# Kernel tuning notes

Hardware: AMD Instinct MI355X
Metric: run time of the kernel (lower is better)

## Reference

```python
import jax, jax.numpy as jnp
import numpy as np

DIM = 768
NUM_HEADS = 8
SCALE = (DIM // NUM_HEADS) ** -0.5  # 96^-0.5, matches head_dim**-0.5
B, N = 8, 4096


def setup_inputs() -> dict:
    key = jax.random.key(0)
    k1, k2 = jax.random.split(key)
    x_1 = jax.random.normal(k1, (B, N, DIM), dtype=jnp.float32)
    x_2 = jax.random.normal(k2, (B, N, DIM), dtype=jnp.float32)
    return {"x_1": x_1, "x_2": x_2}


def reference(x_1, x_2):
    # q = x_1, k = v = x_2; channel-wise (transpose) attention
    # attn[b,c,d] = sum_n q[b,n,c] * k[b,n,d] * scale   -> [B, C, C]
    attn = jnp.einsum('bnc,bnd->bcd', x_1, x_2) * SCALE
    attn = jax.nn.softmax(attn, axis=-1)
    # out[b,c,n] = sum_d attn[b,c,d] * v[b,n,d]          -> [B, C, N]
    return jnp.einsum('bcd,bnd->bcn', attn, x_2)
```

## Files before the change

kernel.cpp:

```cpp
#include <hip/hip_runtime.h>
#include <stdint.h>

typedef _Float16 f16;
typedef _Float16 f16x4 __attribute__((ext_vector_type(4)));
typedef _Float16 f16x8 __attribute__((ext_vector_type(8)));
typedef float f32x4 __attribute__((ext_vector_type(4)));

#define NB 8
#define NN 4096
#define CC 768
#define SCALE_F 0.10206207261596577f

#define GLDS16(gp, lp)                                                       \
  __builtin_amdgcn_global_load_lds(                                          \
      (__attribute__((address_space(1))) void*)(gp),                         \
      (__attribute__((address_space(3))) void*)(lp), 16, 0, 0)

__global__ __launch_bounds__(256) void k_convert(
    const float* __restrict__ x1, const float* __restrict__ x2,
    f16* __restrict__ x1t, f16* __restrict__ x2t, f16* __restrict__ x2b) {
  __shared__ float tile[64][65];
  const int which = blockIdx.z >> 3;
  const int b = blockIdx.z & 7;
  const int n0 = blockIdx.x << 6;
  const int c0 = blockIdx.y << 6;
  const float* src = (which ? x2 : x1) + (size_t)b * NN * CC;
  f16* dt = (which ? x2t : x1t) + (size_t)b * CC * NN;
  const int t = threadIdx.x;
  const int rowi = t >> 4;
  const int col4 = (t & 15) << 2;
#pragma unroll
  for (int it = 0; it < 4; ++it) {
    const int r = it * 16 + rowi;
    const float4 v =
        *reinterpret_cast<const float4*>(&src[(size_t)(n0 + r) * CC + c0 + col4]);
    tile[r][col4 + 0] = v.x;
    tile[r][col4 + 1] = v.y;
    tile[r][col4 + 2] = v.z;
    tile[r][col4 + 3] = v.w;
    if (which) {
      f16x4 o = {(f16)v.x, (f16)v.y, (f16)v.z, (f16)v.w};
      *reinterpret_cast<f16x4*>(
          &x2b[(size_t)b * NN * CC + (size_t)(n0 + r) * CC + c0 + col4]) = o;
    }
  }
  __syncthreads();
  const int c = t >> 2;
  const int nb = (t & 3) << 4;
  f16x8 lo, hi;
#pragma unroll
  for (int j = 0; j < 8; ++j) lo[j] = (f16)tile[nb + j][c];
#pragma unroll
  for (int j = 0; j < 8; ++j) hi[j] = (f16)tile[nb + 8 + j][c];
  f16* o = &dt[(size_t)(c0 + c) * NN + n0 + nb];
  *reinterpret_cast<f16x8*>(o) = lo;
  *reinterpret_cast<f16x8*>(o + 8) = hi;
}

template <bool ATOMIC, int SWZ>
__global__ __launch_bounds__(256) void k_gemm_bt(
    const f16* __restrict__ A, const f16* __restrict__ B,
    float* __restrict__ C, int klen, int lda, int ldb, int ldc,
    size_t sA, size_t sB, size_t sC) {
  __shared__ __align__(16) f16 As[2][128 * 32];
  __shared__ __align__(16) f16 Bs[2][128 * 32];

  const int lin = blockIdx.x;
  const int xcd = lin & 7;
  const int slot = lin >> 3;
  int bx, by, b, ks;
  if (SWZ == 1) {
    b = xcd;
    ks = slot / 36;
    const int item = slot % 36;
    bx = item % 6;
    by = item / 6;
  } else {
    b = xcd;
    ks = 0;
    bx = slot / 6;
    by = slot % 6;
  }

  const f16* Ap = A + (size_t)b * sA + (size_t)by * 128 * lda + (size_t)ks * klen;
  const f16* Bp = B + (size_t)b * sB + (size_t)bx * 128 * ldb + (size_t)ks * klen;
  float* Cp = C + (size_t)b * sC + (size_t)by * 128 * ldc + bx * 128;

  const int tid = threadIdx.x;
  const int wave = tid >> 6;
  const int lane = tid & 63;
  const int wr = wave >> 1;
  const int wc = wave & 1;

  const f16* ga0 = Ap + (size_t)(wave * 32 + (lane >> 2)) * lda + (lane & 3) * 8;
  const f16* ga1 = ga0 + (size_t)16 * lda;
  const f16* gb0 = Bp + (size_t)(wave * 32 + (lane >> 2)) * ldb + (lane & 3) * 8;
  const f16* gb1 = gb0 + (size_t)16 * ldb;
  const int lofs0 = wave * 32 * 32;
  const int lofs1 = lofs0 + 16 * 32;

  const int raofs = (wr * 64 + (lane & 15)) * 32 + (lane >> 4) * 8;
  const int rbofs = (wc * 64 + (lane & 15)) * 32 + (lane >> 4) * 8;

  f32x4 acc[4][4] = {};

  const int nit = klen >> 5;
  GLDS16(ga0, &As[0][lofs0]);
  GLDS16(ga1, &As[0][lofs1]);
  GLDS16(gb0, &Bs[0][lofs0]);
  GLDS16(gb1, &Bs[0][lofs1]);

  for (int it = 0; it < nit; ++it) {
    const int cur = it & 1;
    const int nxt = cur ^ 1;
    __syncthreads();
    if (it + 1 < nit) {
      ga0 += 32; ga1 += 32; gb0 += 32; gb1 += 32;
      GLDS16(ga0, &As[nxt][lofs0]);
      GLDS16(ga1, &As[nxt][lofs1]);
      GLDS16(gb0, &Bs[nxt][lofs0]);
      GLDS16(gb1, &Bs[nxt][lofs1]);
    }
    const f16* ra = &As[cur][raofs];
    const f16* rb = &Bs[cur][rbofs];
    f16x8 af[4], bfv[4];
#pragma unroll
    for (int i = 0; i < 4; ++i)
      af[i] = *reinterpret_cast<const f16x8*>(ra + i * 16 * 32);
#pragma unroll
    for (int j = 0; j < 4; ++j)
      bfv[j] = *reinterpret_cast<const f16x8*>(rb + j * 16 * 32);
#pragma unroll
    for (int i = 0; i < 4; ++i)
#pragma unroll
      for (int j = 0; j < 4; ++j)
        acc[i][j] = __builtin_amdgcn_mfma_f32_16x16x32_f16(af[i], bfv[j],
                                                           acc[i][j], 0, 0, 0);
  }

  const int col = lane & 15;
  const int rq = (lane >> 4) * 4;
#pragma unroll
  for (int i = 0; i < 4; ++i) {
    const int r0 = wr * 64 + i * 16 + rq;
#pragma unroll
    for (int j = 0; j < 4; ++j) {
      const int cidx = wc * 64 + j * 16 + col;
#pragma unroll
      for (int r = 0; r < 4; ++r) {
        const float v = acc[i][j][r];
        if (ATOMIC)
          atomicAdd(&Cp[(size_t)(r0 + r) * ldc + cidx], v);
        else
          Cp[(size_t)(r0 + r) * ldc + cidx] = v;
      }
    }
  }
}

__global__ __launch_bounds__(256) void k_softmax(const float* __restrict__ S,
                                                 f16* __restrict__ P) {
  const int row = blockIdx.x * 4 + (threadIdx.x >> 6);
  const int lane = threadIdx.x & 63;
  const float* s = S + (size_t)row * CC;
  float v[12];
#pragma unroll
  for (int j = 0; j < 3; ++j) {
    const float4 t = *reinterpret_cast<const float4*>(&s[j * 256 + lane * 4]);
    v[j * 4 + 0] = t.x * SCALE_F;
    v[j * 4 + 1] = t.y * SCALE_F;
    v[j * 4 + 2] = t.z * SCALE_F;
    v[j * 4 + 3] = t.w * SCALE_F;
  }
  float m = v[0];
#pragma unroll
  for (int j = 1; j < 12; ++j) m = fmaxf(m, v[j]);
#pragma unroll
  for (int off = 32; off >= 1; off >>= 1) m = fmaxf(m, __shfl_xor(m, off, 64));
  float sum = 0.f;
#pragma unroll
  for (int j = 0; j < 12; ++j) {
    v[j] = __expf(v[j] - m);
    sum += v[j];
  }
#pragma unroll
  for (int off = 32; off >= 1; off >>= 1) sum += __shfl_xor(sum, off, 64);
  const float inv = 1.0f / sum;
  f16* p = P + (size_t)row * CC;
#pragma unroll
  for (int j = 0; j < 3; ++j) {
    f16x4 o = {(f16)(v[j * 4 + 0] * inv), (f16)(v[j * 4 + 1] * inv),
               (f16)(v[j * 4 + 2] * inv), (f16)(v[j * 4 + 3] * inv)};
    *reinterpret_cast<f16x4*>(&p[j * 256 + lane * 4]) = o;
  }
}

extern "C" void kernel_launch(void* const* d_in, const int* in_sizes, int n_in,
                              void* d_out, int out_size, void* d_ws,
                              size_t ws_size, hipStream_t stream) {
  const float* x1 = (const float*)d_in[0];
  const float* x2 = (const float*)d_in[1];
  float* out = (float*)d_out;

  const size_t elems = (size_t)NB * NN * CC;
  f16* x1t = (f16*)d_out;
  f16* x2t = x1t + elems;
  char* ws = (char*)d_ws;
  f16* x2b = (f16*)ws;
  float* S = (float*)(ws + elems * 2);
  f16* P = (f16*)(ws + elems * 2 + (size_t)NB * CC * CC * 4);
  const size_t need =
      elems * 2 + (size_t)NB * CC * CC * 4 + (size_t)NB * CC * CC * 2;
  if (ws_size < need) return;

  k_convert<<<dim3(NN / 64, CC / 64, 2 * NB), 256, 0, stream>>>(x1, x2, x1t,
                                                                x2t, x2b);
  hipMemsetAsync(S, 0, (size_t)NB * CC * CC * 4, stream);
  k_gemm_bt<true, 1><<<dim3(6 * 6 * NB * 4), 256, 0, stream>>>(
      x1t, x2t, S, NN / 4, NN, NN, CC, (size_t)CC * NN, (size_t)CC * NN,
      (size_t)CC * CC);
  k_softmax<<<dim3(NB * CC / 4), 256, 0, stream>>>(S, P);
  k_gemm_bt<false, 2><<<dim3(32 * 6 * NB), 256, 0, stream>>>(
      P, x2b, out, CC, CC, CC, NN, (size_t)CC * CC, (size_t)NN * CC,
      (size_t)CC * NN);
}
```

Before: 419.8 us.

## Triple-buffer GEMM LDS with explicit vmcnt waits and XOR-swizzled layout

Moves the GEMM main loop from double to triple buffering, prefetching two K-tiles ahead. The single __syncthreads is replaced by an explicit s_waitcnt vmcnt plus s_barrier, so loads for later stages can stay in flight while the current tile is consumed. It also XOR-swizzles the 8-element column groups in LDS, applied on both the global-load side and the fragment-read side, to cut bank conflicts. In exchange LDS use grows by half, which may lower occupancy. Correctness now depends on the hand-written vmcnt counts matching the number of outstanding direct-to-LDS loads.

```diff
diff --git a/kernel.cpp b/kernel.cpp
--- a/kernel.cpp
+++ b/kernel.cpp
@@ -62,8 +62,8 @@
     const f16* __restrict__ A, const f16* __restrict__ B,
     float* __restrict__ C, int klen, int lda, int ldb, int ldc,
     size_t sA, size_t sB, size_t sC) {
-  __shared__ __align__(16) f16 As[2][128 * 32];
-  __shared__ __align__(16) f16 Bs[2][128 * 32];
+  __shared__ __align__(16) f16 As[3][128 * 32];
+  __shared__ __align__(16) f16 Bs[3][128 * 32];
 
   const int lin = blockIdx.x;
   const int xcd = lin & 7;
@@ -92,15 +92,20 @@
   const int wr = wave >> 1;
   const int wc = wave & 1;
 
-  const f16* ga0 = Ap + (size_t)(wave * 32 + (lane >> 2)) * lda + (lane & 3) * 8;
+  const int srow = wave * 32 + (lane >> 2);
+  const int scg = ((lane & 3) ^ ((srow >> 1) & 3)) * 8;
+  const f16* ga0 = Ap + (size_t)srow * lda + scg;
   const f16* ga1 = ga0 + (size_t)16 * lda;
-  const f16* gb0 = Bp + (size_t)(wave * 32 + (lane >> 2)) * ldb + (lane & 3) * 8;
+  const f16* gb0 = Bp + (size_t)srow * ldb + scg;
   const f16* gb1 = gb0 + (size_t)16 * ldb;
   const int lofs0 = wave * 32 * 32;
   const int lofs1 = lofs0 + 16 * 32;
 
-  const int raofs = (wr * 64 + (lane & 15)) * 32 + (lane >> 4) * 8;
-  const int rbofs = (wc * 64 + (lane & 15)) * 32 + (lane >> 4) * 8;
+  const int arow = wr * 64 + (lane & 15);
+  const int brow = wc * 64 + (lane & 15);
+  const int kc8 = (lane >> 4) * 8;
+  const int raofs = arow * 32 + (kc8 ^ (((arow >> 1) & 3) * 8));
+  const int rbofs = brow * 32 + (kc8 ^ (((brow >> 1) & 3) * 8));
 
   f32x4 acc[4][4] = {};
 
@@ -109,33 +114,47 @@
   GLDS16(ga1, &As[0][lofs1]);
   GLDS16(gb0, &Bs[0][lofs0]);
   GLDS16(gb1, &Bs[0][lofs1]);
-
+  ga0 += 32; ga1 += 32; gb0 += 32; gb1 += 32;
+  GLDS16(ga0, &As[1][lofs0]);
+  GLDS16(ga1, &As[1][lofs1]);
+  GLDS16(gb0, &Bs[1][lofs0]);
+  GLDS16(gb1, &Bs[1][lofs1]);
+
+  int rb = 0;
+  int wb = 2;
   for (int it = 0; it < nit; ++it) {
-    const int cur = it & 1;
-    const int nxt = cur ^ 1;
-    __syncthreads();
-    if (it + 1 < nit) {
+    if (it + 1 < nit)
+      asm volatile("s_waitcnt vmcnt(4)" ::: "memory");
+    else
+      asm volatile("s_waitcnt vmcnt(0)" ::: "memory");
+    __builtin_amdgcn_s_barrier();
+    __builtin_amdgcn_sched_barrier(0);
+
+    if (it + 2 < nit) {
       ga0 += 32; ga1 += 32; gb0 += 32; gb1 += 32;
-      GLDS16(ga0, &As[nxt][lofs0]);
-      GLDS16(ga1, &As[nxt][lofs1]);
-      GLDS16(gb0, &Bs[nxt][lofs0]);
-      GLDS16(gb1, &Bs[nxt][lofs1]);
+      GLDS16(ga0, &As[wb][lofs0]);
+      GLDS16(ga1, &As[wb][lofs1]);
+      GLDS16(gb0, &Bs[wb][lofs0]);
+      GLDS16(gb1, &Bs[wb][lofs1]);
     }
-    const f16* ra = &As[cur][raofs];
-    const f16* rb = &Bs[cur][rbofs];
+
+    const f16* ra = &As[rb][raofs];
+    const f16* rbp = &Bs[rb][rbofs];
     f16x8 af[4], bfv[4];
 #pragma unroll
     for (int i = 0; i < 4; ++i)
       af[i] = *reinterpret_cast<const f16x8*>(ra + i * 16 * 32);
 #pragma unroll
     for (int j = 0; j < 4; ++j)
-      bfv[j] = *reinterpret_cast<const f16x8*>(rb + j * 16 * 32);
+      bfv[j] = *reinterpret_cast<const f16x8*>(rbp + j * 16 * 32);
 #pragma unroll
     for (int i = 0; i < 4; ++i)
 #pragma unroll
       for (int j = 0; j < 4; ++j)
         acc[i][j] = __builtin_amdgcn_mfma_f32_16x16x32_f16(af[i], bfv[j],
                                                            acc[i][j], 0, 0, 0);
+    rb = (rb == 2) ? 0 : rb + 1;
+    wb = (wb == 2) ? 0 : wb + 1;
   }
 
   const int col = lane & 15;
```

Result: no change. 415.5 us (-1.0%).

## Enlarge GEMM tiles to 256x256x64 with 512 threads and swizzled LDS

Applied to the files above, without the earlier changes.

Both GEMMs move from 128x128 tiles with a K-step of 32 to 256x256 tiles with a K-step of 64, using 8 waves, each computing 128x64. LDS loads use an XOR swizzle to avoid bank conflicts. Staging is now two K-chunks ahead with explicit vmcnt waits and split barriers. The first GEMM's split-K factor drops from 4 to 2, halving atomic traffic. The larger tiles raise data reuse per block, but they shrink the grid (144 and 384 blocks) and use 128KB of LDS, which risks poor occupancy and CU underfill.

```diff
diff --git a/kernel.cpp b/kernel.cpp
--- a/kernel.cpp
+++ b/kernel.cpp
@@ -58,94 +58,122 @@
 }
 
 template <bool ATOMIC, int SWZ>
-__global__ __launch_bounds__(256) void k_gemm_bt(
+__global__ __launch_bounds__(512, 2) void k_gemm_bt(
     const f16* __restrict__ A, const f16* __restrict__ B,
     float* __restrict__ C, int klen, int lda, int ldb, int ldc,
     size_t sA, size_t sB, size_t sC) {
-  __shared__ __align__(16) f16 As[2][128 * 32];
-  __shared__ __align__(16) f16 Bs[2][128 * 32];
+  __shared__ __align__(16) f16 As[2][256 * 64];
+  __shared__ __align__(16) f16 Bs[2][256 * 64];
 
   const int lin = blockIdx.x;
   const int xcd = lin & 7;
   const int slot = lin >> 3;
-  int bx, by, b, ks;
+  int bx, by, ks;
+  const int b = xcd;
   if (SWZ == 1) {
-    b = xcd;
-    ks = slot / 36;
-    const int item = slot % 36;
-    bx = item % 6;
-    by = item / 6;
+    ks = slot / 9;
+    const int item = slot % 9;
+    bx = item % 3;
+    by = item / 3;
   } else {
-    b = xcd;
     ks = 0;
-    bx = slot / 6;
-    by = slot % 6;
-  }
-
-  const f16* Ap = A + (size_t)b * sA + (size_t)by * 128 * lda + (size_t)ks * klen;
-  const f16* Bp = B + (size_t)b * sB + (size_t)bx * 128 * ldb + (size_t)ks * klen;
-  float* Cp = C + (size_t)b * sC + (size_t)by * 128 * ldc + bx * 128;
+    by = slot % 3;
+    bx = slot / 3;
+  }
+
+  const f16* Ap = A + (size_t)b * sA + (size_t)by * 256 * lda + (size_t)ks * klen;
+  const f16* Bp = B + (size_t)b * sB + (size_t)bx * 256 * ldb + (size_t)ks * klen;
+  float* Cp = C + (size_t)b * sC + (size_t)by * 256 * ldc + bx * 256;
 
   const int tid = threadIdx.x;
   const int wave = tid >> 6;
   const int lane = tid & 63;
-  const int wr = wave >> 1;
-  const int wc = wave & 1;
-
-  const f16* ga0 = Ap + (size_t)(wave * 32 + (lane >> 2)) * lda + (lane & 3) * 8;
-  const f16* ga1 = ga0 + (size_t)16 * lda;
-  const f16* gb0 = Bp + (size_t)(wave * 32 + (lane >> 2)) * ldb + (lane & 3) * 8;
-  const f16* gb1 = gb0 + (size_t)16 * ldb;
-  const int lofs0 = wave * 32 * 32;
-  const int lofs1 = lofs0 + 16 * 32;
-
-  const int raofs = (wr * 64 + (lane & 15)) * 32 + (lane >> 4) * 8;
-  const int rbofs = (wc * 64 + (lane & 15)) * 32 + (lane >> 4) * 8;
-
-  f32x4 acc[4][4] = {};
-
-  const int nit = klen >> 5;
-  GLDS16(ga0, &As[0][lofs0]);
-  GLDS16(ga1, &As[0][lofs1]);
-  GLDS16(gb0, &Bs[0][lofs0]);
-  GLDS16(gb1, &Bs[0][lofs1]);
+  const int wr = wave >> 2;
+  const int wn = wave & 3;
+
+  const int srow = lane >> 3;
+  const int ssw = ((lane & 7) ^ srow) * 8;
+  const f16* gA = Ap + (size_t)(wave * 32 + srow) * lda + ssw;
+  const f16* gB = Bp + (size_t)(wave * 32 + srow) * ldb + ssw;
+  const int cb = wave * 4 * 512;
+
+  const int mrow = lane & 15;
+  const int kk = lane >> 4;
+  const int asw = ((kk ^ (mrow & 7)) * 8);
+  const int raofs = (wr * 128 + mrow) * 64 + asw;
+  const int rbofs = (wn * 64 + mrow) * 64 + asw;
+
+  f32x4 acc[8][4] = {};
+
+  const int nit = klen >> 6;
+
+#define STAGE(bufi)                                                          \
+  do {                                                                       \
+    _Pragma("unroll") for (int q = 0; q < 4; ++q) {                          \
+      GLDS16(gA + (size_t)q * 8 * lda, &As[bufi][cb + q * 512]);             \
+      GLDS16(gB + (size_t)q * 8 * ldb, &Bs[bufi][cb + q * 512]);             \
+    }                                                                        \
+  } while (0)
+
+  STAGE(0);
+  gA += 64; gB += 64;
+  STAGE(1);
 
   for (int it = 0; it < nit; ++it) {
-    const int cur = it & 1;
-    const int nxt = cur ^ 1;
-    __syncthreads();
-    if (it + 1 < nit) {
-      ga0 += 32; ga1 += 32; gb0 += 32; gb1 += 32;
-      GLDS16(ga0, &As[nxt][lofs0]);
-      GLDS16(ga1, &As[nxt][lofs1]);
-      GLDS16(gb0, &Bs[nxt][lofs0]);
-      GLDS16(gb1, &Bs[nxt][lofs1]);
+    const int buf = it & 1;
+    if (it + 1 < nit)
+      asm volatile("s_waitcnt vmcnt(8)" ::: "memory");
+    else
+      asm volatile("s_waitcnt vmcnt(0)" ::: "memory");
+    __builtin_amdgcn_s_barrier();
+    __builtin_amdgcn_sched_barrier(0);
+
+    const f16* la = &As[buf][0];
+    const f16* lb = &Bs[buf][0];
+    f16x8 af[8], bf[4];
+#pragma unroll
+    for (int i = 0; i < 8; ++i)
+      af[i] = *reinterpret_cast<const f16x8*>(la + raofs + i * 1024);
+#pragma unroll
+    for (int j = 0; j < 4; ++j)
+      bf[j] = *reinterpret_cast<const f16x8*>(lb + rbofs + j * 1024);
+#pragma unroll
+    for (int i = 0; i < 8; ++i)
+#pragma unroll
+      for (int j = 0; j < 4; ++j)
+        acc[i][j] = __builtin_amdgcn_mfma_f32_16x16x32_f16(af[i], bf[j],
+                                                           acc[i][j], 0, 0, 0);
+#pragma unroll
+    for (int i = 0; i < 8; ++i)
+      af[i] = *reinterpret_cast<const f16x8*>(la + ((raofs + i * 1024) ^ 32));
+#pragma unroll
+    for (int j = 0; j < 4; ++j)
+      bf[j] = *reinterpret_cast<const f16x8*>(lb + ((rbofs + j * 1024) ^ 32));
+    asm volatile("s_waitcnt lgkmcnt(0)" ::: "memory");
+    __builtin_amdgcn_sched_barrier(0);
+    __builtin_amdgcn_s_barrier();
+    __builtin_amdgcn_sched_barrier(0);
+    if (it + 2 < nit) {
+      gA += 64; gB += 64;
+      STAGE(buf);
     }
-    const f16* ra = &As[cur][raofs];
-    const f16* rb = &Bs[cur][rbofs];
-    f16x8 af[4], bfv[4];
-#pragma unroll
-    for (int i = 0; i < 4; ++i)
-      af[i] = *reinterpret_cast<const f16x8*>(ra + i * 16 * 32);
-#pragma unroll
-    for (int j = 0; j < 4; ++j)
-      bfv[j] = *reinterpret_cast<const f16x8*>(rb + j * 16 * 32);
-#pragma unroll
-    for (int i = 0; i < 4; ++i)
+#pragma unroll
+    for (int i = 0; i < 8; ++i)
 #pragma unroll
       for (int j = 0; j < 4; ++j)
-        acc[i][j] = __builtin_amdgcn_mfma_f32_16x16x32_f16(af[i], bfv[j],
+        acc[i][j] = __builtin_amdgcn_mfma_f32_16x16x32_f16(af[i], bf[j],
                                                            acc[i][j], 0, 0, 0);
   }
+#undef STAGE
 
   const int col = lane & 15;
-  const int rq = (lane >> 4) * 4;
-#pragma unroll
-  for (int i = 0; i < 4; ++i) {
-    const int r0 = wr * 64 + i * 16 + rq;
+  const int rq = kk * 4;
+#pragma unroll
+  for (int i = 0; i < 8; ++i) {
+    const int r0 = wr * 128 + i * 16 + rq;
 #pragma unroll
     for (int j = 0; j < 4; ++j) {
-      const int cidx = wc * 64 + j * 16 + col;
+      const int cidx = wn * 64 + j * 16 + col;
 #pragma unroll
       for (int r = 0; r < 4; ++r) {
         const float v = acc[i][j][r];
@@ -216,11 +244,11 @@
   k_convert<<<dim3(NN / 64, CC / 64, 2 * NB), 256, 0, stream>>>(x1, x2, x1t,
                                                                 x2t, x2b);
   hipMemsetAsync(S, 0, (size_t)NB * CC * CC * 4, stream);
-  k_gemm_bt<true, 1><<<dim3(6 * 6 * NB * 4), 256, 0, stream>>>(
-      x1t, x2t, S, NN / 4, NN, NN, CC, (size_t)CC * NN, (size_t)CC * NN,
+  k_gemm_bt<true, 1><<<dim3(9 * NB * 2), 512, 0, stream>>>(
+      x1t, x2t, S, NN / 2, NN, NN, CC, (size_t)CC * NN, (size_t)CC * NN,
       (size_t)CC * CC);
   k_softmax<<<dim3(NB * CC / 4), 256, 0, stream>>>(S, P);
-  k_gemm_bt<false, 2><<<dim3(32 * 6 * NB), 256, 0, stream>>>(
+  k_gemm_bt<false, 2><<<dim3(16 * 3 * NB), 512, 0, stream>>>(
       P, x2b, out, CC, CC, CC, NN, (size_t)CC * CC, (size_t)NN * CC,
       (size_t)CC * NN);
 }
```

Result: no change. 412.2 us (-1.8%).
